# Kernel tuning notes

Measured on AMD Instinct MI355X. Metric: run time of the kernel, lower is better.

Reference implementation:

```python
import jax, jax.numpy as jnp
import numpy as np

K = 8            # NEAREST_K
IN = 68          # input_size = 64 + 4
EO = 32          # edge_output_size
FEAT = IN * 2 + EO * 4  # 264
EMB = 32         # linear_embedding
NCLS = 2
N = 768
EPS = 1e-5


def lrelu(x):
    return jnp.where(x >= 0, x, 0.01 * x)


def setup_inputs() -> dict:
    key = jax.random.key(0)
    ks = jax.random.split(key, 16)

    def w(k, fan_in, fan_out):
        return jax.random.normal(k, (fan_in, fan_out), jnp.float32) / np.float32(np.sqrt(fan_in))

    return {
        "feat0": jax.random.normal(ks[0], (N, IN), jnp.float32),
        "feat1": jax.random.normal(ks[1], (N, IN), jnp.float32),
        # edge_conv1: Linear(IN*K, EO) -> LeakyReLU -> Linear(EO, EO) -> LeakyReLU
        "ec1_w1": w(ks[2], IN * K, EO), "ec1_b1": jnp.zeros((EO,), jnp.float32),
        "ec1_w2": w(ks[3], EO, EO),     "ec1_b2": jnp.zeros((EO,), jnp.float32),
        # edge_conv2: Linear(EO*K, EO) -> LeakyReLU -> Linear(EO, EO) -> LeakyReLU
        "ec2_w1": w(ks[4], EO * K, EO), "ec2_b1": jnp.zeros((EO,), jnp.float32),
        "ec2_w2": w(ks[5], EO, EO),     "ec2_b2": jnp.zeros((EO,), jnp.float32),
        # linear head: BN(FEAT) -> Linear(FEAT,EMB) -> LReLU -> Linear(EMB,EMB) -> LReLU -> Linear(EMB,NCLS)
        "bn_g": jnp.ones((FEAT,), jnp.float32), "bn_b": jnp.zeros((FEAT,), jnp.float32),
        "lin1_w": w(ks[6], FEAT, EMB), "lin1_b": jnp.zeros((EMB,), jnp.float32),
        "lin2_w": w(ks[7], EMB, EMB),  "lin2_b": jnp.zeros((EMB,), jnp.float32),
        "lin3_w": w(ks[8], EMB, NCLS), "lin3_b": jnp.zeros((NCLS,), jnp.float32),
    }


def _pairs_for_graph(feat, ec1_w1, ec1_b1, ec1_w2, ec1_b2,
                     ec2_w1, ec2_b1, ec2_w2, ec2_b2):
    n = feat.shape[0]
    # kNN on first 4 dims via pairwise L1 distance (includes self, dist 0)
    coords = feat[:, :4]
    dist = jnp.abs(coords[:, None, :] - coords[None, :, :]).sum(-1)  # [n, n]
    _, idx = jax.lax.top_k(-dist, K)  # [n, K] smallest distances

    # EdgeConv 1: gather neighbor features, flatten feature-major (matches torch transpose+view)
    e1 = feat[idx]                                  # [n, K, IN]
    e1 = jnp.swapaxes(e1, 1, 2).reshape(n, IN * K)  # [n, IN*K]
    e1 = lrelu(lrelu(e1 @ ec1_w1 + ec1_b1) @ ec1_w2 + ec1_b2)  # [n, EO]

    # EdgeConv 2 on edge1 outputs
    e2 = e1[idx]                                    # [n, K, EO]
    e2 = jnp.swapaxes(e2, 1, 2).reshape(n, EO * K)  # [n, EO*K]
    e2 = lrelu(lrelu(e2 @ ec2_w1 + ec2_b1) @ ec2_w2 + ec2_b2)  # [n, EO]

    x = jnp.concatenate([feat, e1, e2], axis=-1)    # [n, IN + 2*EO] = [n, 132]
    # upper-triangle (i<j) all-pairs concat, row-major order == torch masked_select of triu mask
    iu, ju = jnp.triu_indices(n, k=1)
    return jnp.concatenate([x[iu], x[ju]], axis=-1)  # [n(n-1)/2, FEAT]


def reference(feat0, feat1, ec1_w1, ec1_b1, ec1_w2, ec1_b2,
              ec2_w1, ec2_b1, ec2_w2, ec2_b2,
              bn_g, bn_b, lin1_w, lin1_b, lin2_w, lin2_b, lin3_w, lin3_b):
    ec = (ec1_w1, ec1_b1, ec1_w2, ec1_b2, ec2_w1, ec2_b1, ec2_w2, ec2_b2)
    x = jnp.concatenate([_pairs_for_graph(feat0, *ec),
                         _pairs_for_graph(feat1, *ec)], axis=0)  # [P, FEAT]
    # BatchNorm1d in training mode: batch statistics (biased variance)
    mu = x.mean(axis=0)
    var = x.var(axis=0)
    x = (x - mu) * jax.lax.rsqrt(var + EPS) * bn_g + bn_b
    x = lrelu(x @ lin1_w + lin1_b)
    x = lrelu(x @ lin2_w + lin2_b)
    return x @ lin3_w + lin3_b  # [P, NCLS]
```

## Files before the change

### kernel.cpp

```cpp
#include <hip/hip_runtime.h>

#define NN 768
#define IN_F 68
#define KNN 8
#define EO 32
#define FEAT 264
#define HALF_FEAT 132
#define EMB 32
#define NPAIR 294528

__global__ void __launch_bounds__(64) topk_ec1_kernel(
    const float* __restrict__ feat0, const float* __restrict__ feat1,
    const float* __restrict__ w1, const float* __restrict__ b1,
    const float* __restrict__ w2, const float* __restrict__ b2,
    int* __restrict__ idx_out, float* __restrict__ e1out)
{
  const int i = blockIdx.x, g = blockIdx.y;
  const float* __restrict__ feat = g ? feat1 : feat0;
  const int lane = threadIdx.x;

  __shared__ unsigned long long keys[64*8];
  __shared__ int nbr[8];
  __shared__ float gl[KNN*IN_F];
  __shared__ float hsh[EO];

  const float4 ci = *(const float4*)(feat + i*IN_F);

  float4 cand[12];
#pragma unroll
  for (int t = 0; t < 12; t++)
    cand[t] = *(const float4*)(feat + (lane + 64*t)*IN_F);

  float bd[8]; int bidx[8];
#pragma unroll
  for (int k = 0; k < 8; k++) { bd[k] = 1e30f; bidx[k] = 0; }
#pragma unroll
  for (int t = 0; t < 12; t++) {
    const int j = lane + 64*t;
    float d = fabsf(ci.x - cand[t].x);
    d += fabsf(ci.y - cand[t].y);
    d += fabsf(ci.z - cand[t].z);
    d += fabsf(ci.w - cand[t].w);
    if (d < bd[7]) {
#pragma unroll
      for (int k = 7; k >= 1; k--) {
        if (d < bd[k-1])    { bd[k] = bd[k-1]; bidx[k] = bidx[k-1]; }
        else if (d < bd[k]) { bd[k] = d;       bidx[k] = j; }
      }
      if (d < bd[0]) { bd[0] = d; bidx[0] = j; }
    }
  }
#pragma unroll
  for (int k = 0; k < 8; k++)
    keys[lane*8+k] = ((unsigned long long)__float_as_uint(bd[k]) << 32) | (unsigned)bidx[k];
  __syncthreads();
  int pos = 0;
#pragma unroll
  for (int r = 0; r < 8; r++) {
    unsigned long long mykey = keys[lane*8 + pos];
    unsigned long long mn = mykey;
#pragma unroll
    for (int s = 32; s >= 1; s >>= 1) {
      unsigned long long o = __shfl_xor(mn, s, 64);
      mn = (o < mn) ? o : mn;
    }
    if (mykey == mn) pos++;
    if (lane == 0) {
      int nb = (int)(mn & 0xffffffffull);
      nbr[r] = nb;
      idx_out[(g*NN+i)*8 + r] = nb;
    }
  }
  __syncthreads();

  for (int z = lane; z < KNN*17; z += 64) {
    int k = z / 17, q = z - k*17;
    *(float4*)&gl[k*IN_F + q*4] = *(const float4*)(feat + nbr[k]*IN_F + q*4);
  }
  __syncthreads();

  const int e = lane & 31, hf = lane >> 5;
  float acc = 0.f;
  const int cbeg = hf*34;
  for (int c = cbeg; c < cbeg+34; c++) {
#pragma unroll
    for (int k = 0; k < 8; k++)
      acc += gl[k*IN_F+c] * w1[(c*8+k)*EO + e];
  }
  acc += __shfl_xor(acc, 32, 64);
  if (hf == 0) {
    float h = acc + b1[e];
    hsh[e] = fmaxf(h, 0.01f*h);
  }
  __syncthreads();
  if (lane < 32) {
    float o = b2[lane];
#pragma unroll
    for (int m = 0; m < 32; m++) o += hsh[m] * w2[m*EO + lane];
    o = fmaxf(o, 0.01f*o);
    e1out[(g*NN+i)*EO + lane] = o;
  }
}

__global__ void __launch_bounds__(64) ec2_kernel(
    const int* __restrict__ idx, const float* __restrict__ e1,
    const float* __restrict__ w1, const float* __restrict__ b1,
    const float* __restrict__ w2, const float* __restrict__ b2,
    float* __restrict__ e2out)
{
  const int i = blockIdx.x, g = blockIdx.y;
  const int lane = threadIdx.x;
  __shared__ float gl[KNN*EO];
  __shared__ float hsh[EO];
  {
    const int k = lane >> 3, q = lane & 7;
    const int nb = idx[(g*NN+i)*8 + k];
    *(float4*)&gl[k*EO + q*4] = *(const float4*)(e1 + (g*NN+nb)*EO + q*4);
  }
  __syncthreads();
  const int e = lane & 31, hf = lane >> 5;
  float acc = 0.f;
  const int cbeg = hf*16;
  for (int c = cbeg; c < cbeg+16; c++) {
#pragma unroll
    for (int k = 0; k < 8; k++)
      acc += gl[k*EO+c] * w1[(c*8+k)*EO + e];
  }
  acc += __shfl_xor(acc, 32, 64);
  if (hf == 0) {
    float h = acc + b1[e];
    hsh[e] = fmaxf(h, 0.01f*h);
  }
  __syncthreads();
  if (lane < 32) {
    float o = b2[lane];
#pragma unroll
    for (int m = 0; m < 32; m++) o += hsh[m] * w2[m*EO + lane];
    o = fmaxf(o, 0.01f*o);
    e2out[(g*NN+i)*EO + lane] = o;
  }
}

__global__ void __launch_bounds__(256) stats_kernel(
    const float* __restrict__ feat0, const float* __restrict__ feat1,
    const float* __restrict__ e1, const float* __restrict__ e2,
    const float* __restrict__ bn_g,
    float* __restrict__ mu_out, float* __restrict__ sg_out)
{
  const int c = blockIdx.x;
  const int tid = threadIdx.x;
  double s1=0, s2=0, q1=0, q2=0;
  for (int t = tid; t < 2*NN; t += 256) {
    int g = t >= NN;
    int i = t - g*NN;
    float val;
    if (c < IN_F)      val = (g ? feat1 : feat0)[i*IN_F + c];
    else if (c < 100)  val = e1[(g*NN+i)*EO + (c-IN_F)];
    else               val = e2[(g*NN+i)*EO + (c-100)];
    double dv = val;
    double wf = (double)(NN-1-i), wsnd = (double)i;
    s1 += wf*dv;  s2 += wsnd*dv;
    double dq = dv*dv;
    q1 += wf*dq;  q2 += wsnd*dq;
  }
  __shared__ double sm[256];
  double sums[4] = {s1, s2, q1, q2};
  double tot[4];
#pragma unroll
  for (int z = 0; z < 4; z++) {
    __syncthreads();
    sm[tid] = sums[z];
    __syncthreads();
    for (int off = 128; off >= 1; off >>= 1) {
      if (tid < off) sm[tid] += sm[tid+off];
      __syncthreads();
    }
    tot[z] = sm[0];
  }
  if (tid == 0) {
    const double M2 = 2.0 * (double)NPAIR;
    double mu1 = tot[0]/M2, mu2 = tot[1]/M2;
    double v1 = tot[2]/M2 - mu1*mu1;
    double v2 = tot[3]/M2 - mu2*mu2;
    mu_out[c]           = (float)mu1;
    mu_out[HALF_FEAT+c] = (float)mu2;
    sg_out[c]           = (float)((double)bn_g[c] / sqrt(v1 + 1e-5));
    sg_out[HALF_FEAT+c] = (float)((double)bn_g[HALF_FEAT+c] / sqrt(v2 + 1e-5));
  }
}

__global__ void __launch_bounds__(64) uv_c0_kernel(
    const float* __restrict__ feat0, const float* __restrict__ feat1,
    const float* __restrict__ e1, const float* __restrict__ e2,
    const float* __restrict__ sg, const float* __restrict__ mu,
    const float* __restrict__ bn_b,
    const float* __restrict__ lin1_w, const float* __restrict__ lin1_b,
    float* __restrict__ u, float* __restrict__ v, float* __restrict__ c0g)
{
  const int i = blockIdx.x, g = blockIdx.y;
  const int t = threadIdx.x;
  if (i == NN) {
    if (g == 0 && t < EMB) {
      float acc = lin1_b[t];
      for (int c = 0; c < FEAT; c++)
        acc += (bn_b[c] - mu[c]*sg[c]) * lin1_w[c*EMB + t];
      c0g[t] = acc;
    }
    return;
  }
  __shared__ float x[HALF_FEAT];
  for (int c = t; c < IN_F; c += 64) x[c] = (g ? feat1 : feat0)[i*IN_F + c];
  if (t < 32) x[IN_F + t]     = e1[(g*NN+i)*EO + t];
  else        x[100 + (t-32)] = e2[(g*NN+i)*EO + (t-32)];
  __syncthreads();
  const int e = t & 31, hf = t >> 5;
  const int base = hf * HALF_FEAT;
  float acc = 0.f;
  for (int c = 0; c < HALF_FEAT; c++)
    acc += x[c] * sg[base+c] * lin1_w[(base+c)*EMB + e];
  float* dst = hf ? v : u;
  dst[(g*NN+i)*EMB + e] = acc;
}

__global__ void __launch_bounds__(256) pair_kernel(
    const float* __restrict__ u, const float* __restrict__ v,
    const float* __restrict__ c0g,
    const float* __restrict__ lin2_w, const float* __restrict__ lin2_b,
    const float* __restrict__ lin3_w, const float* __restrict__ lin3_b,
    float2* __restrict__ out)
{
  const int g = blockIdx.y;
  int rem = blockIdx.x;
  int a = 0;
  while (rem >= 48 - a) { rem -= 48 - a; a++; }
  const int b = a + rem;

  __shared__ float su[16*36], sv[16*36];
  const int tid = threadIdx.x;
  {
    int r = tid >> 5, c = tid & 31;
    su[r*36+c] = u[(g*NN + a*16 + r)*EMB + c];
    sv[r*36+c] = v[(g*NN + b*16 + r)*EMB + c];
    r += 8;
    su[r*36+c] = u[(g*NN + a*16 + r)*EMB + c];
    sv[r*36+c] = v[(g*NN + b*16 + r)*EMB + c];
  }
  __syncthreads();

  const int tx = tid & 15, ty = tid >> 4;
  const int i = a*16 + ty, j = b*16 + tx;
  if (j <= i) return;

  float h1[32];
#pragma unroll
  for (int e = 0; e < 32; e++) {
    float s = su[ty*36+e] + sv[tx*36+e] + c0g[e];
    h1[e] = fmaxf(s, 0.01f*s);
  }
  float h2[32];
#pragma unroll
  for (int e = 0; e < 32; e++) h2[e] = lin2_b[e];
#pragma unroll
  for (int m = 0; m < 32; m++) {
    float hm = h1[m];
#pragma unroll
    for (int e = 0; e < 32; e++) h2[e] += hm * lin2_w[m*32+e];
  }
  float o0 = lin3_b[0], o1 = lin3_b[1];
#pragma unroll
  for (int m = 0; m < 32; m++) {
    float h = fmaxf(h2[m], 0.01f*h2[m]);
    o0 += h * lin3_w[m*2+0];
    o1 += h * lin3_w[m*2+1];
  }
  long p = (long)i*NN - (long)i*(i+1)/2 + (j - i - 1);
  out[(long)g*NPAIR + p] = make_float2(o0, o1);
}

extern "C" void kernel_launch(void* const* d_in, const int* in_sizes, int n_in,
                              void* d_out, int out_size, void* d_ws, size_t ws_size,
                              hipStream_t stream)
{
  const float* feat0  = (const float*)d_in[0];
  const float* feat1  = (const float*)d_in[1];
  const float* ec1_w1 = (const float*)d_in[2];
  const float* ec1_b1 = (const float*)d_in[3];
  const float* ec1_w2 = (const float*)d_in[4];
  const float* ec1_b2 = (const float*)d_in[5];
  const float* ec2_w1 = (const float*)d_in[6];
  const float* ec2_b1 = (const float*)d_in[7];
  const float* ec2_w2 = (const float*)d_in[8];
  const float* ec2_b2 = (const float*)d_in[9];
  const float* bn_g   = (const float*)d_in[10];
  const float* bn_b   = (const float*)d_in[11];
  const float* lin1_w = (const float*)d_in[12];
  const float* lin1_b = (const float*)d_in[13];
  const float* lin2_w = (const float*)d_in[14];
  const float* lin2_b = (const float*)d_in[15];
  const float* lin3_w = (const float*)d_in[16];
  const float* lin3_b = (const float*)d_in[17];

  char* ws = (char*)d_ws;
  int*   idx = (int*)  (ws + 0);
  float* e1  = (float*)(ws + 49152);
  float* e2  = (float*)(ws + 245760);
  float* u   = (float*)(ws + 442368);
  float* v   = (float*)(ws + 638976);
  float* mu  = (float*)(ws + 835584);
  float* sg  = (float*)(ws + 836640);
  float* c0g = (float*)(ws + 837696);

  topk_ec1_kernel<<<dim3(768,2), 64, 0, stream>>>(feat0, feat1, ec1_w1, ec1_b1,
                                                  ec1_w2, ec1_b2, idx, e1);
  ec2_kernel<<<dim3(768,2), 64, 0, stream>>>(idx, e1, ec2_w1, ec2_b1,
                                             ec2_w2, ec2_b2, e2);
  stats_kernel<<<dim3(132), 256, 0, stream>>>(feat0, feat1, e1, e2, bn_g, mu, sg);
  uv_c0_kernel<<<dim3(769,2), 64, 0, stream>>>(feat0, feat1, e1, e2, sg, mu, bn_b,
                                               lin1_w, lin1_b, u, v, c0g);
  pair_kernel<<<dim3(1176,2), 256, 0, stream>>>(u, v, c0g, lin2_w, lin2_b,
                                                lin3_w, lin3_b, (float2*)d_out);
}
```

Before: 150.9 us.

## Use split-bf16 MFMA for pair MLP layer and shuffle-based BN reduction

The per-pair 32x32 hidden layer in pair_kernel moves from scalar FP32 FMAs per thread to MFMA 16x16x32 bf16 instructions. Inputs and weights are split into hi/lo bf16 parts and combined in three products to keep near-FP32 accuracy. The layer-3 projection is finished with a shared-memory transpose and cross-lane shuffles. The BN statistics kernel also replaces its shared-memory tree reduction with wavefront shuffles, at the cost of extra bf16 conversion work and LDS traffic per tile.

```diff
diff --git a/kernel.cpp b/kernel.cpp
--- a/kernel.cpp
+++ b/kernel.cpp
@@ -8,6 +8,18 @@
 #define HALF_FEAT 132
 #define EMB 32
 #define NPAIR 294528
+
+typedef __attribute__((ext_vector_type(8))) short bf16x8;
+typedef __attribute__((ext_vector_type(4))) float f32x4;
+
+static __device__ __forceinline__ short f2bf(float x) {
+  unsigned u = __float_as_uint(x);
+  unsigned r = (u + 0x7fffu + ((u >> 16) & 1u)) >> 16;
+  return (short)r;
+}
+static __device__ __forceinline__ float bf2f(short h) {
+  return __uint_as_float(((unsigned)(unsigned short)h) << 16);
+}
 
 __global__ void __launch_bounds__(64) topk_ec1_kernel(
     const float* __restrict__ feat0, const float* __restrict__ feat1,
@@ -163,25 +175,26 @@
     double dq = dv*dv;
     q1 += wf*dq;  q2 += wsnd*dq;
   }
-  __shared__ double sm[256];
-  double sums[4] = {s1, s2, q1, q2};
-  double tot[4];
-#pragma unroll
-  for (int z = 0; z < 4; z++) {
-    __syncthreads();
-    sm[tid] = sums[z];
-    __syncthreads();
-    for (int off = 128; off >= 1; off >>= 1) {
-      if (tid < off) sm[tid] += sm[tid+off];
-      __syncthreads();
-    }
-    tot[z] = sm[0];
-  }
+#pragma unroll
+  for (int off = 32; off >= 1; off >>= 1) {
+    s1 += __shfl_xor(s1, off, 64);
+    s2 += __shfl_xor(s2, off, 64);
+    q1 += __shfl_xor(q1, off, 64);
+    q2 += __shfl_xor(q2, off, 64);
+  }
+  __shared__ double red[4][4];
+  const int w = tid >> 6;
+  if ((tid & 63) == 0) { red[w][0]=s1; red[w][1]=s2; red[w][2]=q1; red[w][3]=q2; }
+  __syncthreads();
   if (tid == 0) {
+    double t0 = red[0][0]+red[1][0]+red[2][0]+red[3][0];
+    double t1 = red[0][1]+red[1][1]+red[2][1]+red[3][1];
+    double t2 = red[0][2]+red[1][2]+red[2][2]+red[3][2];
+    double t3 = red[0][3]+red[1][3]+red[2][3]+red[3][3];
     const double M2 = 2.0 * (double)NPAIR;
-    double mu1 = tot[0]/M2, mu2 = tot[1]/M2;
-    double v1 = tot[2]/M2 - mu1*mu1;
-    double v2 = tot[3]/M2 - mu2*mu2;
+    double mu1 = t0/M2, mu2 = t1/M2;
+    double v1 = t2/M2 - mu1*mu1;
+    double v2 = t3/M2 - mu2*mu2;
     mu_out[c]           = (float)mu1;
     mu_out[HALF_FEAT+c] = (float)mu2;
     sg_out[c]           = (float)((double)bn_g[c] / sqrt(v1 + 1e-5));
@@ -236,6 +249,7 @@
   const int b = a + rem;
 
   __shared__ float su[16*36], sv[16*36];
+  __shared__ float wbuf[4][16*36];
   const int tid = threadIdx.x;
   {
     int r = tid >> 5, c = tid & 31;
@@ -247,34 +261,69 @@
   }
   __syncthreads();
 
-  const int tx = tid & 15, ty = tid >> 4;
-  const int i = a*16 + ty, j = b*16 + tx;
-  if (j <= i) return;
-
-  float h1[32];
-#pragma unroll
-  for (int e = 0; e < 32; e++) {
-    float s = su[ty*36+e] + sv[tx*36+e] + c0g[e];
-    h1[e] = fmaxf(s, 0.01f*s);
-  }
-  float h2[32];
-#pragma unroll
-  for (int e = 0; e < 32; e++) h2[e] = lin2_b[e];
-#pragma unroll
-  for (int m = 0; m < 32; m++) {
-    float hm = h1[m];
-#pragma unroll
-    for (int e = 0; e < 32; e++) h2[e] += hm * lin2_w[m*32+e];
-  }
-  float o0 = lin3_b[0], o1 = lin3_b[1];
-#pragma unroll
-  for (int m = 0; m < 32; m++) {
-    float h = fmaxf(h2[m], 0.01f*h2[m]);
-    o0 += h * lin3_w[m*2+0];
-    o1 += h * lin3_w[m*2+1];
-  }
-  long p = (long)i*NN - (long)i*(i+1)/2 + (j - i - 1);
-  out[(long)g*NPAIR + p] = make_float2(o0, o1);
+  const int lane = tid & 63, w = tid >> 6;
+  const int q = lane & 15, kg = lane >> 4;
+
+  bf16x8 whi0, wlo0, whi1, wlo1;
+#pragma unroll
+  for (int jj = 0; jj < 8; jj++) {
+    float w0 = lin2_w[(kg*8+jj)*32 + q];
+    float w1 = lin2_w[(kg*8+jj)*32 + 16 + q];
+    short h0 = f2bf(w0); whi0[jj] = h0; wlo0[jj] = f2bf(w0 - bf2f(h0));
+    short h1 = f2bf(w1); whi1[jj] = h1; wlo1[jj] = f2bf(w1 - bf2f(h1));
+  }
+  float svc[8];
+#pragma unroll
+  for (int jj = 0; jj < 8; jj++)
+    svc[jj] = sv[q*36 + kg*8 + jj] + c0g[kg*8+jj];
+  float2 w3v[8]; float b2v[8];
+#pragma unroll
+  for (int jj = 0; jj < 8; jj++) {
+    w3v[jj] = ((const float2*)lin3_w)[kg*8+jj];
+    b2v[jj] = lin2_b[kg*8+jj];
+  }
+  const float b30 = lin3_b[0], b31 = lin3_b[1];
+
+  float* wb = wbuf[w];
+#pragma unroll
+  for (int t = 0; t < 4; t++) {
+    const int ty = w*4 + t;
+    bf16x8 ahi, alo;
+#pragma unroll
+    for (int jj = 0; jj < 8; jj++) {
+      float s = su[ty*36 + kg*8 + jj] + svc[jj];
+      s = fmaxf(s, 0.01f*s);
+      short hh = f2bf(s);
+      ahi[jj] = hh; alo[jj] = f2bf(s - bf2f(hh));
+    }
+    f32x4 acc0 = {0.f,0.f,0.f,0.f}, acc1 = {0.f,0.f,0.f,0.f};
+    acc0 = __builtin_amdgcn_mfma_f32_16x16x32_bf16(ahi, whi0, acc0, 0,0,0);
+    acc1 = __builtin_amdgcn_mfma_f32_16x16x32_bf16(ahi, whi1, acc1, 0,0,0);
+    acc0 = __builtin_amdgcn_mfma_f32_16x16x32_bf16(ahi, wlo0, acc0, 0,0,0);
+    acc1 = __builtin_amdgcn_mfma_f32_16x16x32_bf16(ahi, wlo1, acc1, 0,0,0);
+    acc0 = __builtin_amdgcn_mfma_f32_16x16x32_bf16(alo, whi0, acc0, 0,0,0);
+    acc1 = __builtin_amdgcn_mfma_f32_16x16x32_bf16(alo, whi1, acc1, 0,0,0);
+#pragma unroll
+    for (int r = 0; r < 4; r++) {
+      wb[(kg*4+r)*36 + q]      = acc0[r];
+      wb[(kg*4+r)*36 + 16 + q] = acc1[r];
+    }
+    float o0 = 0.f, o1 = 0.f;
+#pragma unroll
+    for (int jj = 0; jj < 8; jj++) {
+      float h = wb[q*36 + kg*8 + jj] + b2v[jj];
+      h = fmaxf(h, 0.01f*h);
+      o0 += h * w3v[jj].x;
+      o1 += h * w3v[jj].y;
+    }
+    o0 += __shfl_xor(o0, 16, 64); o0 += __shfl_xor(o0, 32, 64);
+    o1 += __shfl_xor(o1, 16, 64); o1 += __shfl_xor(o1, 32, 64);
+    const int i = a*16 + ty, j = b*16 + q;
+    if (lane < 16 && j > i) {
+      long p = (long)i*NN - (long)i*(i+1)/2 + (j - i - 1);
+      out[(long)g*NPAIR + p] = make_float2(o0 + b30, o1 + b31);
+    }
+  }
 }
 
 extern "C" void kernel_launch(void* const* d_in, const int* in_sizes, int n_in,
```

New measurement: 139.2 us. 1.08x faster.
